# Optimization experiments

Hardware: AMD Instinct MI355X
Metric: run time of the kernel (lower is better)

The kernel has to match this reference:

```python
import jax, jax.numpy as jnp
import numpy as np

N_NODES = 100000
N_EDGES = 1600000
F_IN = 128
F_OUT = 64


def setup_inputs() -> dict:
    key = jax.random.key(0)
    k0, k1, k2, k3, k4, k5 = jax.random.split(key, 6)
    stdv = 1.0 / np.sqrt(F_OUT)
    x = jax.random.normal(k0, (N_NODES, F_IN), dtype=jnp.float32)
    edge_src = jax.random.randint(k1, (N_EDGES,), 0, N_NODES, dtype=jnp.int32)
    edge_dst = jax.random.randint(k2, (N_EDGES,), 0, N_NODES, dtype=jnp.int32)
    # normalized adjacency values (all positive, like D^-1/2 A D^-1/2 entries)
    edge_weight = jax.random.uniform(k3, (N_EDGES,), dtype=jnp.float32)
    weight = jax.random.uniform(k4, (F_IN, F_OUT), dtype=jnp.float32, minval=-stdv, maxval=stdv)
    bias = jax.random.uniform(k5, (F_OUT,), dtype=jnp.float32, minval=-stdv, maxval=stdv)
    return {"x": x, "edge_weight": edge_weight, "weight": weight, "bias": bias,
            "edge_src": edge_src, "edge_dst": edge_dst}


def reference(x, edge_weight, weight, bias, edge_src, edge_dst):
    # support = X @ W  -- dense GEMM [N, F_in] x [F_in, F_out]
    support = x @ weight
    # spmm(adj, support): adj in COO form; gather source rows, scale by edge value,
    # scatter-add into destination rows.
    msgs = support[edge_src] * edge_weight[:, None]          # [E, F_out]
    out = jax.ops.segment_sum(msgs, edge_dst, num_segments=x.shape[0])
    return out + bias
```

## Files before the change

### kernel.cpp

```cpp
#include <hip/hip_runtime.h>
#include <hip/hip_bf16.h>

#define F_IN 128
#define F_OUT 64
#define BUCKET_SHIFT 7
#define BUCKET_NODES 128
#define BUCKET_CAP 2880
#define CNT_STRIDE 16
#define NB_MAX 800
#define SCAT_CHUNK 8192
#define GEMM_ROWS 64
#define LDK 136

typedef __attribute__((ext_vector_type(8))) short bf16x8;
typedef __attribute__((ext_vector_type(4))) float f32x4;

__device__ inline short bf16_bits(float f) {
  __hip_bfloat16 h = __float2bfloat16(f);
  return *reinterpret_cast<short*>(&h);
}

__global__ __launch_bounds__(256) void gcn_gemm_mfma_kernel(
    const float* __restrict__ x, const float* __restrict__ w,
    __hip_bfloat16* __restrict__ support, int n_nodes) {
  __shared__ short As[GEMM_ROWS][LDK];
  __shared__ short Bs[F_OUT][LDK];
  const int tid = threadIdx.x;
  const int block_row = blockIdx.x * GEMM_ROWS;

#pragma unroll
  for (int i = 0; i < F_IN * F_OUT / 256; ++i) {
    const int idx = tid + i * 256;
    const int k = idx >> 6;
    const int n = idx & 63;
    Bs[n][k] = bf16_bits(w[idx]);
  }
#pragma unroll
  for (int i = 0; i < GEMM_ROWS * F_IN / 4 / 256; ++i) {
    const int idx = tid + i * 256;
    const int row = idx >> 5;
    const int c4 = idx & 31;
    float4 v = make_float4(0.f, 0.f, 0.f, 0.f);
    if (block_row + row < n_nodes)
      v = ((const float4*)(x + (size_t)(block_row + row) * F_IN))[c4];
    short4 b;
    b.x = bf16_bits(v.x);
    b.y = bf16_bits(v.y);
    b.z = bf16_bits(v.z);
    b.w = bf16_bits(v.w);
    *(short4*)&As[row][c4 * 4] = b;
  }
  __syncthreads();

  const int lane = tid & 63;
  const int wid = tid >> 6;
  const int wr0 = wid * 16;
  const int m = lane & 15;
  const int quad = lane >> 4;

  f32x4 acc0 = {0.f, 0.f, 0.f, 0.f};
  f32x4 acc1 = {0.f, 0.f, 0.f, 0.f};
  f32x4 acc2 = {0.f, 0.f, 0.f, 0.f};
  f32x4 acc3 = {0.f, 0.f, 0.f, 0.f};
#pragma unroll
  for (int ks = 0; ks < 4; ++ks) {
    const int ko = ks * 32 + quad * 8;
    const bf16x8 a  = *(const bf16x8*)&As[wr0 + m][ko];
    const bf16x8 b0 = *(const bf16x8*)&Bs[0 + m][ko];
    const bf16x8 b1 = *(const bf16x8*)&Bs[16 + m][ko];
    const bf16x8 b2 = *(const bf16x8*)&Bs[32 + m][ko];
    const bf16x8 b3 = *(const bf16x8*)&Bs[48 + m][ko];
    acc0 = __builtin_amdgcn_mfma_f32_16x16x32_bf16(a, b0, acc0, 0, 0, 0);
    acc1 = __builtin_amdgcn_mfma_f32_16x16x32_bf16(a, b1, acc1, 0, 0, 0);
    acc2 = __builtin_amdgcn_mfma_f32_16x16x32_bf16(a, b2, acc2, 0, 0, 0);
    acc3 = __builtin_amdgcn_mfma_f32_16x16x32_bf16(a, b3, acc3, 0, 0, 0);
  }
#pragma unroll
  for (int r = 0; r < 4; ++r) {
    const int row = block_row + wr0 + quad * 4 + r;
    if (row < n_nodes) {
      __hip_bfloat16* op = support + (size_t)row * F_OUT;
      op[0 + m]  = __float2bfloat16(acc0[r]);
      op[16 + m] = __float2bfloat16(acc1[r]);
      op[32 + m] = __float2bfloat16(acc2[r]);
      op[48 + m] = __float2bfloat16(acc3[r]);
    }
  }
}

__global__ __launch_bounds__(512) void gcn_bucket_scatter_kernel(
    const int* __restrict__ esrc, const int* __restrict__ edst,
    const float* __restrict__ ew, int* __restrict__ bcount,
    int2* __restrict__ region, int n_edges, int nb) {
  __shared__ int lhist[NB_MAX];
  __shared__ int lcur[NB_MAX];
  __shared__ int ldst_cache[SCAT_CHUNK];
  const int e0 = blockIdx.x * SCAT_CHUNK;
  const int e1 = min(e0 + SCAT_CHUNK, n_edges);
  const int n_local = e1 - e0;

  for (int i = threadIdx.x; i < nb; i += 512) lhist[i] = 0;
  __syncthreads();
  for (int i = threadIdx.x; i < n_local; i += 512) {
    const int d = edst[e0 + i];
    ldst_cache[i] = d;
    atomicAdd(&lhist[d >> BUCKET_SHIFT], 1);
  }
  __syncthreads();
  for (int b = threadIdx.x; b < nb; b += 512) {
    const int c = lhist[b];
    lcur[b] = c ? atomicAdd(&bcount[b * CNT_STRIDE], c) : 0;
  }
  __syncthreads();
  for (int i = threadIdx.x; i < n_local; i += 512) {
    const int d = ldst_cache[i];
    const int b = d >> BUCKET_SHIFT;
    const int pos = atomicAdd(&lcur[b], 1);
    if (pos < BUCKET_CAP) {
      region[(size_t)b * BUCKET_CAP + pos] =
          make_int2((esrc[e0 + i] << BUCKET_SHIFT) | (d & (BUCKET_NODES - 1)),
                    __float_as_int(ew[e0 + i]));
    }
  }
}

__global__ __launch_bounds__(1024) void gcn_bucket_scan_kernel(
    const int* __restrict__ bcount, int* __restrict__ bbase, int nb) {
  __shared__ int wtot[16];
  const int lane = threadIdx.x & 63;
  const int wid = threadIdx.x >> 6;
  int c = 0;
  if (threadIdx.x < nb) {
    c = bcount[threadIdx.x * CNT_STRIDE];
    c = (c < BUCKET_CAP ? c : BUCKET_CAP);
  }
  int s = c;
#pragma unroll
  for (int off = 1; off < 64; off <<= 1) {
    const int t = __shfl_up(s, off, 64);
    if (lane >= off) s += t;
  }
  if (lane == 63) wtot[wid] = s;
  __syncthreads();
  if (wid == 0) {
    const int wv = (lane < 16) ? wtot[lane] : 0;
    int wsc = wv;
#pragma unroll
    for (int off = 1; off < 16; off <<= 1) {
      const int t = __shfl_up(wsc, off, 64);
      if (lane >= off) wsc += t;
    }
    if (lane < 16) wtot[lane] = wsc - wv;
  }
  __syncthreads();
  if (threadIdx.x < nb) bbase[threadIdx.x] = (s - c) + wtot[wid];
}

__global__ __launch_bounds__(256) void gcn_bucket_sort_kernel(
    const int2* __restrict__ region, const int* __restrict__ bcount,
    const int* __restrict__ bbase, int2* __restrict__ sorted,
    int* __restrict__ ends, int n_nodes) {
  __shared__ int2 eb[BUCKET_CAP];
  __shared__ int2 outb[BUCKET_CAP];
  __shared__ int lhist[BUCKET_NODES];
  __shared__ int lcur[BUCKET_NODES];
  const int b = blockIdx.x;
  int cnt = bcount[b * CNT_STRIDE];
  cnt = (cnt < BUCKET_CAP ? cnt : BUCKET_CAP);
  const int gbase = bbase[b];
  const int node0 = b << BUCKET_SHIFT;

  for (int i = threadIdx.x; i < BUCKET_NODES; i += 256) lhist[i] = 0;
  __syncthreads();
  for (int i = threadIdx.x; i < cnt; i += 256) {
    const int2 p = region[(size_t)b * BUCKET_CAP + i];
    eb[i] = p;
    atomicAdd(&lhist[p.x & (BUCKET_NODES - 1)], 1);
  }
  __syncthreads();
  const int lane = threadIdx.x & 63;
  if (threadIdx.x < 64) {
    const int v0 = lhist[lane];
    const int v1 = lhist[64 + lane];
    int s0 = v0;
#pragma unroll
    for (int off = 1; off < 64; off <<= 1) {
      const int t = __shfl_up(s0, off, 64);
      if (lane >= off) s0 += t;
    }
    const int tot0 = __shfl(s0, 63, 64);
    int s1 = v1;
#pragma unroll
    for (int off = 1; off < 64; off <<= 1) {
      const int t = __shfl_up(s1, off, 64);
      if (lane >= off) s1 += t;
    }
    s1 += tot0;
    lcur[lane] = s0 - v0;
    lcur[64 + lane] = s1 - v1;
    const int n0 = node0 + lane;
    const int n1 = node0 + 64 + lane;
    if (n0 < n_nodes) ends[n0] = gbase + s0;
    if (n1 < n_nodes) ends[n1] = gbase + s1;
  }
  __syncthreads();
  for (int i = threadIdx.x; i < cnt; i += 256) {
    const int2 p = eb[i];
    const int ldst = p.x & (BUCKET_NODES - 1);
    const int pos = atomicAdd(&lcur[ldst], 1);
    outb[pos] = make_int2(p.x >> BUCKET_SHIFT, p.y);
  }
  __syncthreads();
  for (int i = threadIdx.x; i < cnt; i += 256) {
    sorted[gbase + i] = outb[i];
  }
}

__global__ __launch_bounds__(256) void gcn_aggregate_kernel(
    const __hip_bfloat16* __restrict__ support, const int2* __restrict__ sorted,
    const int* __restrict__ ends, const float* __restrict__ bias,
    float* __restrict__ out, int n_nodes) {
  const int node = (blockIdx.x * 256 + threadIdx.x) >> 6;
  const int lane = threadIdx.x & 63;
  if (node >= n_nodes) return;
  const int start = (node == 0) ? 0 : ends[node - 1];
  const int end = ends[node];
  float acc = 0.f;
  for (int base = start; base < end; base += 64) {
    const int m = end - base;
    int2 meta = make_int2(0, 0);
    if (lane < m) meta = sorted[base + lane];
    const int m4 = (m < 64 ? m : 64);
    const int mr = (m4 + 7) & ~7;
    for (int j = 0; j < mr; j += 8) {
      int sidx[8];
      float wv[8];
#pragma unroll
      for (int u = 0; u < 8; ++u) {
        sidx[u] = __shfl(meta.x, j + u, 64);
        wv[u] = __int_as_float(__shfl(meta.y, j + u, 64));
      }
      float v[8];
#pragma unroll
      for (int u = 0; u < 8; ++u)
        v[u] = __bfloat162float(support[(size_t)sidx[u] * F_OUT + lane]);
#pragma unroll
      for (int u = 0; u < 8; ++u) acc += v[u] * wv[u];
    }
  }
  out[(size_t)node * F_OUT + lane] = acc + bias[lane];
}

extern "C" void kernel_launch(void* const* d_in, const int* in_sizes, int n_in,
                              void* d_out, int out_size, void* d_ws, size_t ws_size,
                              hipStream_t stream) {
  const float* x    = (const float*)d_in[0];
  const float* ew   = (const float*)d_in[1];
  const float* w    = (const float*)d_in[2];
  const float* bias = (const float*)d_in[3];
  const int*   esrc = (const int*)d_in[4];
  const int*   edst = (const int*)d_in[5];
  float* out = (float*)d_out;

  const int n_nodes = in_sizes[0] / F_IN;
  const int n_edges = in_sizes[4];
  const int nb = (n_nodes + BUCKET_NODES - 1) >> BUCKET_SHIFT;

  char* ws = (char*)d_ws;
  int2* sorted = (int2*)ws;
  ws += ((size_t)n_edges * sizeof(int2) + 255) / 256 * 256;
  int* ends = (int*)ws;
  ws += ((size_t)n_nodes * sizeof(int) + 255) / 256 * 256;
  int* bcount = (int*)ws;
  const size_t bcount_bytes = (size_t)nb * CNT_STRIDE * sizeof(int);
  ws += (bcount_bytes + 255) / 256 * 256;
  int* bbase = (int*)ws;
  ws += ((size_t)nb * sizeof(int) + 255) / 256 * 256;
  int2* region = (int2*)ws;
  __hip_bfloat16* support = (__hip_bfloat16*)ws;

  hipMemsetAsync(bcount, 0, bcount_bytes, stream);
  gcn_bucket_scatter_kernel<<<(n_edges + SCAT_CHUNK - 1) / SCAT_CHUNK, 512, 0,
                              stream>>>(esrc, edst, ew, bcount, region, n_edges,
                                        nb);
  gcn_bucket_scan_kernel<<<1, 1024, 0, stream>>>(bcount, bbase, nb);
  gcn_bucket_sort_kernel<<<nb, 256, 0, stream>>>(region, bcount, bbase, sorted,
                                                 ends, n_nodes);
  gcn_gemm_mfma_kernel<<<(n_nodes + GEMM_ROWS - 1) / GEMM_ROWS, 256, 0,
                         stream>>>(x, w, support, n_nodes);
  gcn_aggregate_kernel<<<(n_nodes * 64 + 255) / 256, 256, 0, stream>>>(
      support, sorted, ends, bias, out, n_nodes);
}
```

Baseline: 209.7 us.

## Fuse bucket scan into sort kernel and process four nodes per wave in aggregation

The separate single-block scan launch is removed. Each sort block now computes its own global base by summing the clamped counts of all preceding buckets with a block reduction. The aggregation kernel now assigns four consecutive destination nodes to each wave and shares one sliding 64-entry metadata window across them. This cuts per-node window loads and padding waste for low-degree nodes. The cost is redundant prefix reads in the sort kernel (quadratic in the number of buckets, but small) and fewer waves in flight during aggregation.

```diff
diff --git a/kernel.cpp b/kernel.cpp
--- a/kernel.cpp
+++ b/kernel.cpp
@@ -11,6 +11,7 @@
 #define SCAT_CHUNK 8192
 #define GEMM_ROWS 64
 #define LDK 136
+#define NODES_PER_WAVE 4
 
 typedef __attribute__((ext_vector_type(8))) short bf16x8;
 typedef __attribute__((ext_vector_type(4))) float f32x4;
@@ -124,62 +125,44 @@
   }
 }
 
-__global__ __launch_bounds__(1024) void gcn_bucket_scan_kernel(
-    const int* __restrict__ bcount, int* __restrict__ bbase, int nb) {
-  __shared__ int wtot[16];
-  const int lane = threadIdx.x & 63;
-  const int wid = threadIdx.x >> 6;
-  int c = 0;
-  if (threadIdx.x < nb) {
-    c = bcount[threadIdx.x * CNT_STRIDE];
-    c = (c < BUCKET_CAP ? c : BUCKET_CAP);
-  }
-  int s = c;
-#pragma unroll
-  for (int off = 1; off < 64; off <<= 1) {
-    const int t = __shfl_up(s, off, 64);
-    if (lane >= off) s += t;
-  }
-  if (lane == 63) wtot[wid] = s;
-  __syncthreads();
-  if (wid == 0) {
-    const int wv = (lane < 16) ? wtot[lane] : 0;
-    int wsc = wv;
-#pragma unroll
-    for (int off = 1; off < 16; off <<= 1) {
-      const int t = __shfl_up(wsc, off, 64);
-      if (lane >= off) wsc += t;
-    }
-    if (lane < 16) wtot[lane] = wsc - wv;
-  }
-  __syncthreads();
-  if (threadIdx.x < nb) bbase[threadIdx.x] = (s - c) + wtot[wid];
-}
-
 __global__ __launch_bounds__(256) void gcn_bucket_sort_kernel(
     const int2* __restrict__ region, const int* __restrict__ bcount,
-    const int* __restrict__ bbase, int2* __restrict__ sorted,
-    int* __restrict__ ends, int n_nodes) {
+    int2* __restrict__ sorted, int* __restrict__ ends, int n_nodes, int nb) {
   __shared__ int2 eb[BUCKET_CAP];
   __shared__ int2 outb[BUCKET_CAP];
   __shared__ int lhist[BUCKET_NODES];
   __shared__ int lcur[BUCKET_NODES];
+  __shared__ int red[4];
+  __shared__ int s_gbase;
   const int b = blockIdx.x;
+  const int tid = threadIdx.x;
+  const int lane = tid & 63;
+  const int wid = tid >> 6;
+
+  int psum = 0;
+  for (int i = tid; i < b; i += 256) {
+    int c = bcount[i * CNT_STRIDE];
+    psum += (c < BUCKET_CAP ? c : BUCKET_CAP);
+  }
+#pragma unroll
+  for (int off = 32; off >= 1; off >>= 1) psum += __shfl_down(psum, off, 64);
+  if (lane == 0) red[wid] = psum;
+
   int cnt = bcount[b * CNT_STRIDE];
   cnt = (cnt < BUCKET_CAP ? cnt : BUCKET_CAP);
-  const int gbase = bbase[b];
   const int node0 = b << BUCKET_SHIFT;
 
-  for (int i = threadIdx.x; i < BUCKET_NODES; i += 256) lhist[i] = 0;
-  __syncthreads();
-  for (int i = threadIdx.x; i < cnt; i += 256) {
+  for (int i = tid; i < BUCKET_NODES; i += 256) lhist[i] = 0;
+  __syncthreads();
+  if (tid == 0) s_gbase = red[0] + red[1] + red[2] + red[3];
+  for (int i = tid; i < cnt; i += 256) {
     const int2 p = region[(size_t)b * BUCKET_CAP + i];
     eb[i] = p;
     atomicAdd(&lhist[p.x & (BUCKET_NODES - 1)], 1);
   }
   __syncthreads();
-  const int lane = threadIdx.x & 63;
-  if (threadIdx.x < 64) {
+  const int gbase = s_gbase;
+  if (tid < 64) {
     const int v0 = lhist[lane];
     const int v1 = lhist[64 + lane];
     int s0 = v0;
@@ -204,14 +187,14 @@
     if (n1 < n_nodes) ends[n1] = gbase + s1;
   }
   __syncthreads();
-  for (int i = threadIdx.x; i < cnt; i += 256) {
+  for (int i = tid; i < cnt; i += 256) {
     const int2 p = eb[i];
     const int ldst = p.x & (BUCKET_NODES - 1);
     const int pos = atomicAdd(&lcur[ldst], 1);
     outb[pos] = make_int2(p.x >> BUCKET_SHIFT, p.y);
   }
   __syncthreads();
-  for (int i = threadIdx.x; i < cnt; i += 256) {
+  for (int i = tid; i < cnt; i += 256) {
     sorted[gbase + i] = outb[i];
   }
 }
@@ -219,36 +202,66 @@
 __global__ __launch_bounds__(256) void gcn_aggregate_kernel(
     const __hip_bfloat16* __restrict__ support, const int2* __restrict__ sorted,
     const int* __restrict__ ends, const float* __restrict__ bias,
-    float* __restrict__ out, int n_nodes) {
-  const int node = (blockIdx.x * 256 + threadIdx.x) >> 6;
+    float* __restrict__ out, int n_nodes, int n_edges) {
+  const int wave = (blockIdx.x * 256 + threadIdx.x) >> 6;
   const int lane = threadIdx.x & 63;
-  if (node >= n_nodes) return;
-  const int start = (node == 0) ? 0 : ends[node - 1];
-  const int end = ends[node];
-  float acc = 0.f;
-  for (int base = start; base < end; base += 64) {
-    const int m = end - base;
-    int2 meta = make_int2(0, 0);
-    if (lane < m) meta = sorted[base + lane];
-    const int m4 = (m < 64 ? m : 64);
-    const int mr = (m4 + 7) & ~7;
-    for (int j = 0; j < mr; j += 8) {
-      int sidx[8];
-      float wv[8];
-#pragma unroll
-      for (int u = 0; u < 8; ++u) {
-        sidx[u] = __shfl(meta.x, j + u, 64);
-        wv[u] = __int_as_float(__shfl(meta.y, j + u, 64));
+  const int n0 = wave * NODES_PER_WAVE;
+  if (n0 >= n_nodes) return;
+
+  const int seg_lo = (n0 == 0) ? 0 : ends[n0 - 1];
+  int ek = 0;
+  if (lane < NODES_PER_WAVE) {
+    const int ni = n0 + lane;
+    ek = ends[ni < n_nodes ? ni : n_nodes - 1];
+  }
+  int ends4[NODES_PER_WAVE];
+#pragma unroll
+  for (int k = 0; k < NODES_PER_WAVE; ++k) ends4[k] = __shfl(ek, k, 64);
+
+  int winbase = seg_lo;
+  int2 meta = make_int2(0, 0);
+  if (winbase + lane < n_edges) meta = sorted[winbase + lane];
+
+  const float bv = bias[lane];
+  int segstart = seg_lo;
+#pragma unroll
+  for (int k = 0; k < NODES_PER_WAVE; ++k) {
+    const int node = n0 + k;
+    if (node >= n_nodes) break;
+    const int segend = ends4[k];
+    float acc = 0.f;
+    int j = segstart;
+    while (j < segend) {
+      if (j - winbase >= 64) {
+        winbase += 64;
+        meta = make_int2(0, 0);
+        if (winbase + lane < n_edges) meta = sorted[winbase + lane];
       }
-      float v[8];
-#pragma unroll
-      for (int u = 0; u < 8; ++u)
-        v[u] = __bfloat162float(support[(size_t)sidx[u] * F_OUT + lane]);
-#pragma unroll
-      for (int u = 0; u < 8; ++u) acc += v[u] * wv[u];
-    }
-  }
-  out[(size_t)node * F_OUT + lane] = acc + bias[lane];
+      const int lim = min(segend, winbase + 64);
+      for (; j < lim; j += 8) {
+        int sidx[8];
+        float wv[8];
+#pragma unroll
+        for (int u = 0; u < 8; ++u) {
+          const int jj = j + u;
+          const bool valid = jj < lim;
+          const int idx = valid ? (jj - winbase) : 0;
+          sidx[u] = __shfl(meta.x, idx, 64);
+          const float wraw = __int_as_float(__shfl(meta.y, idx, 64));
+          wv[u] = valid ? wraw : 0.f;
+        }
+        float v[8];
+#pragma unroll
+        for (int u = 0; u < 8; ++u)
+          v[u] = __bfloat162float(support[(size_t)sidx[u] * F_OUT + lane]);
+#pragma unroll
+        for (int u = 0; u < 8; ++u) acc += v[u] * wv[u];
+      }
+      j = lim;
+    }
+    out[(size_t)node * F_OUT + lane] = acc + bv;
+    segstart = segend;
+  }
 }
 
 extern "C" void kernel_launch(void* const* d_in, const int* in_sizes, int n_in,
@@ -274,8 +287,6 @@
   int* bcount = (int*)ws;
   const size_t bcount_bytes = (size_t)nb * CNT_STRIDE * sizeof(int);
   ws += (bcount_bytes + 255) / 256 * 256;
-  int* bbase = (int*)ws;
-  ws += ((size_t)nb * sizeof(int) + 255) / 256 * 256;
   int2* region = (int2*)ws;
   __hip_bfloat16* support = (__hip_bfloat16*)ws;
 
@@ -283,11 +294,11 @@
   gcn_bucket_scatter_kernel<<<(n_edges + SCAT_CHUNK - 1) / SCAT_CHUNK, 512, 0,
                               stream>>>(esrc, edst, ew, bcount, region, n_edges,
                                         nb);
-  gcn_bucket_scan_kernel<<<1, 1024, 0, stream>>>(bcount, bbase, nb);
-  gcn_bucket_sort_kernel<<<nb, 256, 0, stream>>>(region, bcount, bbase, sorted,
-                                                 ends, n_nodes);
+  gcn_bucket_sort_kernel<<<nb, 256, 0, stream>>>(region, bcount, sorted, ends,
+                                                 n_nodes, nb);
   gcn_gemm_mfma_kernel<<<(n_nodes + GEMM_ROWS - 1) / GEMM_ROWS, 256, 0,
                          stream>>>(x, w, support, n_nodes);
-  gcn_aggregate_kernel<<<(n_nodes * 64 + 255) / 256, 256, 0, stream>>>(
-      support, sorted, ends, bias, out, n_nodes);
-}
+  const int nwaves = (n_nodes + NODES_PER_WAVE - 1) / NODES_PER_WAVE;
+  gcn_aggregate_kernel<<<(nwaves * 64 + 255) / 256, 256, 0, stream>>>(
+      support, sorted, ends, bias, out, n_nodes, n_edges);
+}
```

New measurement: 216.8 us. 1.03x slower.
